# Optimization experiments

Hardware: AMD Instinct MI355X
Metric: run time of the kernel (lower is better)

Reference implementation:

```python
import jax, jax.numpy as jnp
import numpy as np

B, T, C, HS = 4, 2048, 1024, 128

def setup_inputs() -> dict:
    key = jax.random.key(0)
    k0, k1, k2, k3 = jax.random.split(key, 4)
    scale = 1.0 / np.sqrt(C)
    return {
        "x": jax.random.normal(k0, (B, T, C), dtype=jnp.float32),
        "Wk": jax.random.normal(k1, (C, HS), dtype=jnp.float32) * scale,
        "Wq": jax.random.normal(k2, (C, HS), dtype=jnp.float32) * scale,
        "Wv": jax.random.normal(k3, (C, HS), dtype=jnp.float32) * scale,
    }

def reference(x, Wk, Wq, Wv):
    # k, q, v: [B, T, HS]
    k = jnp.einsum('btc,ch->bth', x, Wk)
    q = jnp.einsum('btc,ch->bth', x, Wq)
    v = jnp.einsum('btc,ch->bth', x, Wv)
    hs = k.shape[-1]
    # full T x T scores (no causal mask in source), scaled by head_size**-0.5
    wei = jnp.einsum('bqh,bkh->bqk', q, k) * (hs ** -0.5)
    wei = jax.nn.softmax(wei, axis=-1)
    # dropout p=0.0 -> identity
    out = jnp.einsum('bqk,bkh->bqh', wei, v)
    return out
```

## Files before the change

kernel.cpp:

```cpp
#include <hip/hip_runtime.h>
#include <hip/hip_bf16.h>

typedef float  f32x4  __attribute__((ext_vector_type(4)));
typedef float  f32x8  __attribute__((ext_vector_type(8)));
typedef float  f32x16 __attribute__((ext_vector_type(16)));
typedef short  s4v    __attribute__((ext_vector_type(4)));
typedef short  s8v    __attribute__((ext_vector_type(8)));
typedef __bf16 b4v    __attribute__((ext_vector_type(4)));
typedef __bf16 b8v    __attribute__((ext_vector_type(8)));
typedef unsigned int u32;
typedef unsigned short ushort;

#define T_DIM  2048
#define C_DIM  1024


typedef const __attribute__((address_space(1))) u32 gu32;
typedef __attribute__((address_space(3))) u32 lu32;

static __device__ __forceinline__ void glds16(const void* g, void* l) {
  __builtin_amdgcn_global_load_lds((gu32*)g, (lu32*)l, 16, 0, 0);
}

static __device__ __forceinline__ b8v ldb8(const ushort* p) {
  return __builtin_bit_cast(b8v, *reinterpret_cast<const s8v*>(p));
}

static __device__ __forceinline__ b4v cvt4(f32x4 v) {
  b4v r;
#pragma unroll
  for (int i = 0; i < 4; ++i) r[i] = (__bf16)v[i];
  return r;
}

static __device__ __forceinline__ ushort bfu(float f) {
  __bf16 h = (__bf16)f;
  return __builtin_bit_cast(ushort, h);
}

static __device__ __forceinline__ f32x16 mfma32(b8v a, b8v b, f32x16 c) {
  return __builtin_amdgcn_mfma_f32_32x32x16_bf16(a, b, c, 0, 0, 0);
}

#define BAR_VM(N)                                                        \
  asm volatile("s_waitcnt vmcnt(" #N ") lgkmcnt(0)" ::: "memory");       \
  __builtin_amdgcn_s_barrier();                                          \
  asm volatile("" ::: "memory");

__global__ __launch_bounds__(256) void wconv(const float* __restrict__ Wq,
                                             const float* __restrict__ Wk,
                                             const float* __restrict__ Wv,
                                             ushort* __restrict__ Wt) {
  __shared__ float lds[32][65];
  const int m  = blockIdx.z;
  const int c0 = blockIdx.x * 32;
  const int h0 = blockIdx.y * 64;
  const float* W = (m == 0) ? Wq : (m == 1) ? Wk : Wv;

  const int cl = threadIdx.x >> 3;
  const int h8 = (threadIdx.x & 7) * 8;
  {
    float4 a = *reinterpret_cast<const float4*>(W + (c0 + cl) * 128 + h0 + h8);
    float4 b =
        *reinterpret_cast<const float4*>(W + (c0 + cl) * 128 + h0 + h8 + 4);
    lds[cl][h8] = a.x; lds[cl][h8 + 1] = a.y;
    lds[cl][h8 + 2] = a.z; lds[cl][h8 + 3] = a.w;
    lds[cl][h8 + 4] = b.x; lds[cl][h8 + 5] = b.y;
    lds[cl][h8 + 6] = b.z; lds[cl][h8 + 7] = b.w;
  }
  __syncthreads();
  const int hl = threadIdx.x >> 2;
  const int cs = (threadIdx.x & 3) * 8;
  s8v o;
#pragma unroll
  for (int i = 0; i < 8; ++i) o[i] = (short)bfu(lds[cs + i][hl]);
  *reinterpret_cast<s8v*>(Wt + (m * 128 + h0 + hl) * C_DIM + c0 + cs) = o;
}

__global__ __launch_bounds__(512) void proj(const float* __restrict__ x,
                                            const ushort* __restrict__ Wt,
                                            ushort* __restrict__ q,
                                            ushort* __restrict__ k,
                                            ushort* __restrict__ vt) {
  __shared__ __align__(16) ushort Ab[2][32 * 72];
  __shared__ __align__(16) ushort Bb[2][128 * 64];
  float* red = (float*)&Bb[0][0];
  ushort* stage = &Bb[1][0];

  const int t   = threadIdx.x;
  const int w   = t >> 6;
  const int lid = t & 63;
  const int hi  = lid >> 5;
  const int ln  = lid & 31;
  const int ks  = w >> 2;
  const int nc  = w & 3;
  const int m   = blockIdx.y;
  const int r0  = blockIdx.x * 32;

  const int arow = t >> 4;
  const int acol = (t & 15) * 4;
  const float* ag = x + (r0 + arow) * C_DIM + acol;

  const int bswz = (((lid & 7) ^ (lid >> 3)) << 4);
  const char* bg = (const char*)(Wt + m * 128 * C_DIM);

  f32x16 acc[2] = {};

#define PROJ_BSTAGE(KK, BUF)                                              \
  _Pragma("unroll") for (int j = 0; j < 2; ++j) {                         \
    int h = j * 64 + w * 8 + (lid >> 3);                                  \
    glds16(bg + h * 2048 + (KK) * 2 + bswz,                               \
           (char*)&Bb[BUF][0] + j * 8192 + w * 1024);                     \
  }

  f32x4 av = *reinterpret_cast<const f32x4*>(ag);
  PROJ_BSTAGE(0, 0)
  {
    b4v ac = cvt4(av);
    *reinterpret_cast<s4v*>(&Ab[0][arow * 72 + acol]) =
        __builtin_bit_cast(s4v, ac);
  }
  __syncthreads();

  int cur = 0;
#pragma unroll 1
  for (int i = 0; i < 16; ++i) {
    const int nxt = cur ^ 1;
    f32x4 an;
    if (i < 15) {
      const int kk = (i + 1) * 64;
      PROJ_BSTAGE(kk, nxt)
      an = *reinterpret_cast<const f32x4*>(ag + kk);
    }

    const int h = nc * 32 + ln;
#pragma unroll
    for (int c = 0; c < 2; ++c) {
      const int s = ks * 2 + c;
      b8v af = ldb8(&Ab[cur][ln * 72 + s * 16 + hi * 8]);
      int inner = ((s * 2 + hi) << 4) ^ ((h & 7) << 4);
      b8v bf =
          ldb8((const ushort*)((const char*)&Bb[cur][0] + h * 128 + inner));
      __builtin_amdgcn_s_setprio(1);
      acc[c] = mfma32(af, bf, acc[c]);
      __builtin_amdgcn_s_setprio(0);
    }

    if (i < 15) {
      b4v anc = cvt4(an);
      *reinterpret_cast<s4v*>(&Ab[nxt][arow * 72 + acol]) =
          __builtin_bit_cast(s4v, anc);
    }
    __syncthreads();
    cur = nxt;
  }
#undef PROJ_BSTAGE

  f32x16 fa = acc[0] + acc[1];

  if (ks == 1) {
#pragma unroll
    for (int r = 0; r < 16; ++r) {
      int qm = (r & 3) + 8 * (r >> 2) + 4 * hi;
      red[(nc * 32 + qm) * 32 + ln] = fa[r];
    }
  }
  __syncthreads();
  if (ks == 0) {
#pragma unroll
    for (int r = 0; r < 16; ++r) {
      int qm = (r & 3) + 8 * (r >> 2) + 4 * hi;
      fa[r] += red[(nc * 32 + qm) * 32 + ln];
    }
    if (m < 2) {
#pragma unroll
      for (int r = 0; r < 16; ++r) {
        int row = (r & 3) + 8 * (r >> 2) + 4 * hi;
        stage[row * 136 + nc * 32 + ln] = bfu(fa[r]);
      }
    } else {
#pragma unroll
      for (int r = 0; r < 16; ++r) {
        int trow = (r & 3) + 8 * (r >> 2) + 4 * hi;
        stage[(nc * 32 + ln) * 40 + trow] = bfu(fa[r]);
      }
    }
  }
  __syncthreads();

  if (m < 2) {
    ushort* dst = (m == 0) ? q : k;
    int row = t >> 4, col8 = t & 15;
    s8v v8 = *reinterpret_cast<const s8v*>(&stage[row * 136 + col8 * 8]);
    *reinterpret_cast<s8v*>(&dst[(r0 + row) * 128 + col8 * 8]) = v8;
  } else {
    int b = blockIdx.x >> 6;
    int tbase = (blockIdx.x & 63) * 32;
    int h2 = t >> 2, t8 = t & 3;
    s8v v8 = *reinterpret_cast<const s8v*>(&stage[h2 * 40 + t8 * 8]);
    *reinterpret_cast<s8v*>(&vt[(b * 128 + h2) * T_DIM + tbase + t8 * 8]) = v8;
  }
}

#define ATTN_STAGE(KV0, BUF)                                              \
  _Pragma("unroll") for (int j = 0; j < 4; ++j) {                         \
    int row = w * 16 + j * 4 + (lid >> 4);                                \
    int p_ = (row >> 2) & 7;                                              \
    int pg = (p_ & 4) | ((p_ & 1) << 1) | ((p_ >> 1) & 1);                \
    int srow = (row & ~31) | (pg << 2) | (row & 3);                       \
    glds16(kgb + ((KV0) + srow) * 256 + (((lid & 15) ^ (row & 15)) << 4), \
           smem + (BUF) * 65536 + w * 4096 + j * 1024);                   \
  }                                                                       \
  _Pragma("unroll") for (int j = 0; j < 4; ++j) {                         \
    int h = w * 16 + j * 4 + (lid >> 4);                                  \
    glds16(vgb + h * 4096 + (KV0) * 2 + (((lid & 15) ^ (h & 15)) << 4),   \
           smem + (BUF) * 65536 + 32768 + w * 4096 + j * 1024);           \
  }

#define ATTN2_QK(BUF)                                                    \
  {                                                                      \
    const char* Tb = smem + (BUF) * 65536;                               \
    b8v kfr[8];                                                          \
    _Pragma("unroll") for (int s = 0; s < 8; ++s)                        \
        kfr[s] = ldb8((const ushort*)(Tb + koff[s]));                    \
    f32x16 S = {};                                                       \
    __builtin_amdgcn_s_setprio(1);                                       \
    _Pragma("unroll") for (int s = 0; s < 8; ++s)                        \
        S = mfma32(kfr[s], aq[s], S);                                    \
    __builtin_amdgcn_s_setprio(0);                                       \
    float p[16];                                                         \
    _Pragma("unroll") for (int r = 0; r < 16; ++r) {                     \
      p[r] = __expf(S[r] * scale - 4.0f);                                \
      lsum += p[r];                                                      \
    }                                                                    \
    _Pragma("unroll") for (int r = 0; r < 8; ++r) {                      \
      pk0[r] = (__bf16)p[r];                                             \
      pk1[r] = (__bf16)p[8 + r];                                         \
    }                                                                    \
  }

#define ATTN2_PV(BUF)                                                   \
  {                                                                     \
    const char* Tb = smem + (BUF) * 65536;                              \
    __builtin_amdgcn_s_setprio(1);                                      \
    _Pragma("unroll") for (int ht = 0; ht < 4; ++ht) {                  \
      b8v v0 = ldb8((const ushort*)(Tb + voff[ht][0]));                 \
      b8v v1 = ldb8((const ushort*)(Tb + voff[ht][1]));                 \
      of[ht] = mfma32(pk0, v0, of[ht]);                                 \
      of[ht] = mfma32(pk1, v1, of[ht]);                                 \
    }                                                                   \
    __builtin_amdgcn_s_setprio(0);                                      \
  }

__global__ __launch_bounds__(512) void attn2(const ushort* __restrict__ q,
                                             const ushort* __restrict__ k,
                                             const ushort* __restrict__ vt,
                                             float* __restrict__ out,
                                             float* __restrict__ parts,
                                             float* __restrict__ lps) {
  extern __shared__ __align__(16) char smem[];

  const int t   = threadIdx.x;
  const int w   = t >> 6;
  const int lid = t & 63;
  const int hi  = lid >> 5;
  const int ln  = lid & 31;
  const int wq  = w >> 2;
  const int wk  = w & 3;

  const int id = blockIdx.x;
  const int g  = id & 7;
  const int b  = g >> 1;
  const int z  = g & 1;
  const int t0 = (id >> 3) * 64;

  const ushort* qp = q + (b * T_DIM + t0 + wq * 32) * 128;
  b8v aq[8];
#pragma unroll
  for (int s = 0; s < 8; ++s)
    aq[s] = ldb8(&qp[ln * 128 + s * 16 + hi * 8]);

  const char* kgb = (const char*)(k + b * T_DIM * 128);
  const char* vgb = (const char*)(vt + b * 128 * T_DIM);
  const int kv_base = z * 1024;

  const int R = wk * 32 + ln;
  int koff[8];
#pragma unroll
  for (int s = 0; s < 8; ++s)
    koff[s] = R * 256 + (((s * 2 + hi) ^ (R & 15)) << 4);
  int voff[4][2];
#pragma unroll
  for (int ht = 0; ht < 4; ++ht)
#pragma unroll
    for (int s = 0; s < 2; ++s) {
      int Hrow = ht * 32 + ln;
      int chunk = wk * 4 + s * 2 + hi;
      voff[ht][s] = 32768 + Hrow * 256 + ((chunk ^ (Hrow & 15)) << 4);
    }

  f32x16 of[4] = {};
  float lsum = 0.0f;
  b8v pk0, pk1;
  const float scale = 0.08838834764831845f;

  ATTN_STAGE(kv_base, 0)

#pragma unroll 1
  for (int i = 0; i < 7; ++i) {
    BAR_VM(4)
    ATTN_STAGE(kv_base + (i + 1) * 128, (i + 1) & 1)
    ATTN2_QK(i & 1)
    BAR_VM(8)
    ATTN2_PV(i & 1)
  }
  BAR_VM(4)
  ATTN2_QK(1)
  BAR_VM(0)
  ATTN2_PV(1)

  lsum += __shfl_xor(lsum, 32);

  __syncthreads();

  float* ob = (float*)smem;
  float* lb = (float*)(smem + 98304);

  if (lid < 32) lb[(wq * 4 + wk) * 32 + lid] = lsum;
  if (wk != 0) {
#pragma unroll
    for (int ht = 0; ht < 4; ++ht)
#pragma unroll
      for (int r = 0; r < 16; ++r) {
        int qm = (r & 3) + 8 * (r >> 2) + 4 * hi;
        ob[((wk - 1) * 64 + wq * 32 + qm) * 128 + ht * 32 + ln] = of[ht][r];
      }
  }
  __syncthreads();
  if (wk == 0) {
    float* dsto = (z == 0) ? out : parts;
#pragma unroll
    for (int ht = 0; ht < 4; ++ht)
#pragma unroll
      for (int r = 0; r < 16; ++r) {
        int qm = (r & 3) + 8 * (r >> 2) + 4 * hi;
        int row = wq * 32 + qm;
        int col = ht * 32 + ln;
        float val = of[ht][r] + ob[(0 * 64 + row) * 128 + col] +
                    ob[(1 * 64 + row) * 128 + col] +
                    ob[(2 * 64 + row) * 128 + col];
        dsto[(b * T_DIM + t0 + row) * 128 + col] = val;
      }
    if (lid < 32) {
      float lt = lb[(wq * 4 + 0) * 32 + lid] + lb[(wq * 4 + 1) * 32 + lid] +
                 lb[(wq * 4 + 2) * 32 + lid] + lb[(wq * 4 + 3) * 32 + lid];
      lps[z * 8192 + b * T_DIM + t0 + wq * 32 + lid] = lt;
    }
  }
}

__global__ __launch_bounds__(512) void attn3(const ushort* __restrict__ q,
                                             const ushort* __restrict__ k,
                                             const ushort* __restrict__ vt,
                                             float* __restrict__ out,
                                             float* __restrict__ parts,
                                             float* __restrict__ lps) {
  extern __shared__ __align__(16) char smem[];

  const int t   = threadIdx.x;
  const int w   = t >> 6;
  const int lid = t & 63;
  const int hi  = lid >> 5;
  const int ln  = lid & 31;
  const int wq  = w >> 2;
  const int wh  = (w >> 1) & 1;
  const int wk  = w & 1;
  const int b   = blockIdx.y;
  const int z   = blockIdx.z;
  const int t0  = blockIdx.x * 64;

  const ushort* qp = q + (b * T_DIM + t0 + wq * 32) * 128;
  b8v aq[8];
#pragma unroll
  for (int s = 0; s < 8; ++s)
    aq[s] = ldb8(&qp[ln * 128 + s * 16 + hi * 8]);

  const char* kgb = (const char*)(k + b * T_DIM * 128);
  const char* vgb = (const char*)(vt + b * 128 * T_DIM);
  const int kv_base = z * 512;

  const int R = wk * 32 + ln;
  int koff[8];
#pragma unroll
  for (int s = 0; s < 8; ++s)
    koff[s] = R * 256 + (((s * 2 + hi) ^ (R & 15)) << 4);
  int voff[2][2];
#pragma unroll
  for (int ht = 0; ht < 2; ++ht)
#pragma unroll
    for (int s = 0; s < 2; ++s) {
      int Hrow = wh * 64 + ht * 32 + ln;
      int chunk = wk * 4 + s * 2 + hi;
      voff[ht][s] = 16384 + Hrow * 128 + ((chunk ^ (Hrow & 7)) << 4);
    }

  f32x16 of[2] = {};
  float lsum = 0.0f;
  b8v pk0, pk1;
  const float scale = 0.08838834764831845f;

#define A3_STAGE(KV0, BUF)                                                \
  _Pragma("unroll") for (int j = 0; j < 2; ++j) {                         \
    int row = (w * 2 + j) * 4 + (lid >> 4);                               \
    int p_ = (row >> 2) & 7;                                              \
    int pg = (p_ & 4) | ((p_ & 1) << 1) | ((p_ >> 1) & 1);                \
    int srow = (row & ~31) | (pg << 2) | (row & 3);                       \
    glds16(kgb + ((KV0) + srow) * 256 + (((lid & 15) ^ (row & 15)) << 4), \
           smem + (BUF) * 32768 + (w * 2 + j) * 1024);                    \
  }                                                                       \
  _Pragma("unroll") for (int j = 0; j < 2; ++j) {                         \
    int h = (w * 2 + j) * 8 + (lid >> 3);                                 \
    glds16(vgb + h * 4096 + (KV0) * 2 + (((lid & 7) ^ (h & 7)) << 4),     \
           smem + (BUF) * 32768 + 16384 + (w * 2 + j) * 1024);            \
  }

#define A3_QK(BUF)                                                       \
  {                                                                      \
    const char* Tb = smem + (BUF) * 32768;                               \
    b8v kfr[8];                                                          \
    _Pragma("unroll") for (int s = 0; s < 8; ++s)                        \
        kfr[s] = ldb8((const ushort*)(Tb + koff[s]));                    \
    f32x16 S = {};                                                       \
    __builtin_amdgcn_s_setprio(1);                                       \
    _Pragma("unroll") for (int s = 0; s < 8; ++s)                        \
        S = mfma32(kfr[s], aq[s], S);                                    \
    __builtin_amdgcn_s_setprio(0);                                       \
    float p[16];                                                         \
    _Pragma("unroll") for (int r = 0; r < 16; ++r) {                     \
      p[r] = __expf(S[r] * scale - 4.0f);                                \
      lsum += p[r];                                                      \
    }                                                                    \
    _Pragma("unroll") for (int r = 0; r < 8; ++r) {                      \
      pk0[r] = (__bf16)p[r];                                             \
      pk1[r] = (__bf16)p[8 + r];                                         \
    }                                                                    \
  }

#define A3_PV(BUF)                                                      \
  {                                                                     \
    const char* Tb = smem + (BUF) * 32768;                              \
    __builtin_amdgcn_s_setprio(1);                                      \
    _Pragma("unroll") for (int ht = 0; ht < 2; ++ht) {                  \
      b8v v0 = ldb8((const ushort*)(Tb + voff[ht][0]));                 \
      b8v v1 = ldb8((const ushort*)(Tb + voff[ht][1]));                 \
      of[ht] = mfma32(pk0, v0, of[ht]);                                 \
      of[ht] = mfma32(pk1, v1, of[ht]);                                 \
    }                                                                   \
    __builtin_amdgcn_s_setprio(0);                                      \
  }

  A3_STAGE(kv_base, 0)

#pragma unroll 1
  for (int i = 0; i < 7; ++i) {
    BAR_VM(2)
    A3_STAGE(kv_base + (i + 1) * 64, (i + 1) & 1)
    A3_QK(i & 1)
    BAR_VM(4)
    A3_PV(i & 1)
  }
  BAR_VM(2)
  A3_QK(1)
  BAR_VM(0)
  A3_PV(1)

#undef A3_STAGE
#undef A3_QK
#undef A3_PV

  lsum += __shfl_xor(lsum, 32);

  __syncthreads();

  float* ob = (float*)smem;
  float* lb = (float*)(smem + 32768);

  if (wh == 0 && lid < 32) lb[(wk * 2 + wq) * 32 + lid] = lsum;
  if (wk == 1) {
#pragma unroll
    for (int ht = 0; ht < 2; ++ht)
#pragma unroll
      for (int r = 0; r < 16; ++r) {
        int qm = (r & 3) + 8 * (r >> 2) + 4 * hi;
        ob[(wq * 2 + wh) * 2048 + qm * 64 + ht * 32 + ln] = of[ht][r];
      }
  }
  __syncthreads();
  if (wk == 0) {
    float* dsto = (z == 0) ? out : (parts + (z - 1) * 1048576);
#pragma unroll
    for (int ht = 0; ht < 2; ++ht)
#pragma unroll
      for (int r = 0; r < 16; ++r) {
        int qm = (r & 3) + 8 * (r >> 2) + 4 * hi;
        int row = wq * 32 + qm;
        int col = wh * 64 + ht * 32 + ln;
        float val = of[ht][r] + ob[(wq * 2 + wh) * 2048 + qm * 64 + ht * 32 + ln];
        dsto[(b * T_DIM + t0 + row) * 128 + col] = val;
      }
    if (wh == 0 && lid < 32) {
      float lt = lb[(0 * 2 + wq) * 32 + lid] + lb[(1 * 2 + wq) * 32 + lid];
      lps[z * 8192 + b * T_DIM + t0 + wq * 32 + lid] = lt;
    }
  }
}

__global__ __launch_bounds__(256) void fin(float* __restrict__ out,
                                           const float* __restrict__ parts,
                                           const float* __restrict__ lps,
                                           int nz) {
  int tid = blockIdx.x * 256 + threadIdx.x;
  int idx = tid * 4;
  int row = idx >> 7;
  float l = lps[row];
  for (int zz = 1; zz < nz; ++zz) l += lps[zz * 8192 + row];
  float inv = 1.0f / l;
  f32x4 a = *reinterpret_cast<const f32x4*>(out + idx);
  for (int zz = 1; zz < nz; ++zz) {
    f32x4 c = *reinterpret_cast<const f32x4*>(parts + (zz - 1) * 1048576 + idx);
    a += c;
  }
  f32x4 r;
#pragma unroll
  for (int i = 0; i < 4; ++i) r[i] = a[i] * inv;
  *reinterpret_cast<f32x4*>(out + idx) = r;
}

extern "C" void kernel_launch(void* const* d_in, const int* in_sizes, int n_in,
                              void* d_out, int out_size, void* d_ws,
                              size_t ws_size, hipStream_t stream) {
  const float* x  = (const float*)d_in[0];
  const float* Wk = (const float*)d_in[1];
  const float* Wq = (const float*)d_in[2];
  const float* Wv = (const float*)d_in[3];
  float* out = (float*)d_out;

  char* ws = (char*)d_ws;
  ushort* Wt  = (ushort*)ws;
  ushort* qb  = (ushort*)(ws + 786432);
  ushort* kb  = (ushort*)(ws + 2883584);
  ushort* vtb = (ushort*)(ws + 4980736);
  float* parts = (float*)(ws + 7077888);

  const bool big = ws_size >= 19800000u;
  float* lps = big ? (float*)(ws + 7077888 + 3u * 4194304u)
                   : (float*)(ws + 7077888 + 4194304u);

  (void)hipFuncSetAttribute(reinterpret_cast<const void*>(&attn2),
                            hipFuncAttributeMaxDynamicSharedMemorySize, 131072);
  (void)hipFuncSetAttribute(reinterpret_cast<const void*>(&attn3),
                            hipFuncAttributeMaxDynamicSharedMemorySize, 65536);

  wconv<<<dim3(32, 2, 3), dim3(256), 0, stream>>>(Wq, Wk, Wv, Wt);
  proj<<<dim3(256, 3), dim3(512), 0, stream>>>(x, Wt, qb, kb, vtb);
  if (big) {
    attn3<<<dim3(32, 4, 4), dim3(512), 65536, stream>>>(qb, kb, vtb, out,
                                                        parts, lps);
    fin<<<dim3(1024), dim3(256), 0, stream>>>(out, parts, lps, 4);
  } else {
    attn2<<<dim3(256), dim3(512), 131072, stream>>>(qb, kb, vtb, out,
                                                    parts, lps);
    fin<<<dim3(1024), dim3(256), 0, stream>>>(out, parts, lps, 2);
  }
}
```

Before: 55.11 us.

## Store split-KV partials as bf16 and simplify attention pipeline waits

```diff
diff --git a/kernel.cpp b/kernel.cpp
--- a/kernel.cpp
+++ b/kernel.cpp
@@ -36,6 +36,11 @@
 static __device__ __forceinline__ ushort bfu(float f) {
   __bf16 h = (__bf16)f;
   return __builtin_bit_cast(ushort, h);
+}
+
+static __device__ __forceinline__ float b2f(ushort u) {
+  u32 x = ((u32)u) << 16;
+  return __builtin_bit_cast(float, x);
 }
 
 static __device__ __forceinline__ f32x16 mfma32(b8v a, b8v b, f32x16 c) {
@@ -217,7 +222,58 @@
            smem + (BUF) * 65536 + 32768 + w * 4096 + j * 1024);           \
   }
 
-#define ATTN2_QK(BUF)                                                    \
+__global__ __launch_bounds__(512) void attn2(const ushort* __restrict__ q,
+                                             const ushort* __restrict__ k,
+                                             const ushort* __restrict__ vt,
+                                             float* __restrict__ out,
+                                             float* __restrict__ parts,
+                                             float* __restrict__ lps) {
+  extern __shared__ __align__(16) char smem[];
+
+  const int t   = threadIdx.x;
+  const int w   = t >> 6;
+  const int lid = t & 63;
+  const int hi  = lid >> 5;
+  const int ln  = lid & 31;
+  const int wq  = w >> 2;
+  const int wk  = w & 3;
+
+  const int id = blockIdx.x;
+  const int g  = id & 7;
+  const int b  = g >> 1;
+  const int z  = g & 1;
+  const int t0 = (id >> 3) * 64;
+
+  const ushort* qp = q + (b * T_DIM + t0 + wq * 32) * 128;
+  b8v aq[8];
+#pragma unroll
+  for (int s = 0; s < 8; ++s)
+    aq[s] = ldb8(&qp[ln * 128 + s * 16 + hi * 8]);
+
+  const char* kgb = (const char*)(k + b * T_DIM * 128);
+  const char* vgb = (const char*)(vt + b * 128 * T_DIM);
+  const int kv_base = z * 1024;
+
+  const int R = wk * 32 + ln;
+  int koff[8];
+#pragma unroll
+  for (int s = 0; s < 8; ++s)
+    koff[s] = R * 256 + (((s * 2 + hi) ^ (R & 15)) << 4);
+  int voff[4][2];
+#pragma unroll
+  for (int ht = 0; ht < 4; ++ht)
+#pragma unroll
+    for (int s = 0; s < 2; ++s) {
+      int Hrow = ht * 32 + ln;
+      int chunk = wk * 4 + s * 2 + hi;
+      voff[ht][s] = 32768 + Hrow * 256 + ((chunk ^ (Hrow & 15)) << 4);
+    }
+
+  f32x16 of[4] = {};
+  float lsum = 0.0f;
+  const float scale = 0.08838834764831845f;
+
+#define ATTN2_BODY(BUF)                                                  \
   {                                                                      \
     const char* Tb = smem + (BUF) * 65536;                               \
     b8v kfr[8];                                                          \
@@ -233,91 +289,30 @@
       p[r] = __expf(S[r] * scale - 4.0f);                                \
       lsum += p[r];                                                      \
     }                                                                    \
+    b8v pk0, pk1;                                                        \
     _Pragma("unroll") for (int r = 0; r < 8; ++r) {                      \
       pk0[r] = (__bf16)p[r];                                             \
       pk1[r] = (__bf16)p[8 + r];                                         \
     }                                                                    \
-  }
-
-#define ATTN2_PV(BUF)                                                   \
-  {                                                                     \
-    const char* Tb = smem + (BUF) * 65536;                              \
-    __builtin_amdgcn_s_setprio(1);                                      \
-    _Pragma("unroll") for (int ht = 0; ht < 4; ++ht) {                  \
-      b8v v0 = ldb8((const ushort*)(Tb + voff[ht][0]));                 \
-      b8v v1 = ldb8((const ushort*)(Tb + voff[ht][1]));                 \
-      of[ht] = mfma32(pk0, v0, of[ht]);                                 \
-      of[ht] = mfma32(pk1, v1, of[ht]);                                 \
-    }                                                                   \
-    __builtin_amdgcn_s_setprio(0);                                      \
-  }
-
-__global__ __launch_bounds__(512) void attn2(const ushort* __restrict__ q,
-                                             const ushort* __restrict__ k,
-                                             const ushort* __restrict__ vt,
-                                             float* __restrict__ out,
-                                             float* __restrict__ parts,
-                                             float* __restrict__ lps) {
-  extern __shared__ __align__(16) char smem[];
-
-  const int t   = threadIdx.x;
-  const int w   = t >> 6;
-  const int lid = t & 63;
-  const int hi  = lid >> 5;
-  const int ln  = lid & 31;
-  const int wq  = w >> 2;
-  const int wk  = w & 3;
-
-  const int id = blockIdx.x;
-  const int g  = id & 7;
-  const int b  = g >> 1;
-  const int z  = g & 1;
-  const int t0 = (id >> 3) * 64;
-
-  const ushort* qp = q + (b * T_DIM + t0 + wq * 32) * 128;
-  b8v aq[8];
-#pragma unroll
-  for (int s = 0; s < 8; ++s)
-    aq[s] = ldb8(&qp[ln * 128 + s * 16 + hi * 8]);
-
-  const char* kgb = (const char*)(k + b * T_DIM * 128);
-  const char* vgb = (const char*)(vt + b * 128 * T_DIM);
-  const int kv_base = z * 1024;
-
-  const int R = wk * 32 + ln;
-  int koff[8];
-#pragma unroll
-  for (int s = 0; s < 8; ++s)
-    koff[s] = R * 256 + (((s * 2 + hi) ^ (R & 15)) << 4);
-  int voff[4][2];
-#pragma unroll
-  for (int ht = 0; ht < 4; ++ht)
-#pragma unroll
-    for (int s = 0; s < 2; ++s) {
-      int Hrow = ht * 32 + ln;
-      int chunk = wk * 4 + s * 2 + hi;
-      voff[ht][s] = 32768 + Hrow * 256 + ((chunk ^ (Hrow & 15)) << 4);
-    }
-
-  f32x16 of[4] = {};
-  float lsum = 0.0f;
-  b8v pk0, pk1;
-  const float scale = 0.08838834764831845f;
+    __builtin_amdgcn_s_setprio(1);                                       \
+    _Pragma("unroll") for (int ht = 0; ht < 4; ++ht) {                   \
+      b8v v0 = ldb8((const ushort*)(Tb + voff[ht][0]));                  \
+      b8v v1 = ldb8((const ushort*)(Tb + voff[ht][1]));                  \
+      of[ht] = mfma32(pk0, v0, of[ht]);                                  \
+      of[ht] = mfma32(pk1, v1, of[ht]);                                  \
+    }                                                                    \
+    __builtin_amdgcn_s_setprio(0);                                       \
+  }
 
   ATTN_STAGE(kv_base, 0)
 
 #pragma unroll 1
-  for (int i = 0; i < 7; ++i) {
-    BAR_VM(4)
-    ATTN_STAGE(kv_base + (i + 1) * 128, (i + 1) & 1)
-    ATTN2_QK(i & 1)
-    BAR_VM(8)
-    ATTN2_PV(i & 1)
-  }
-  BAR_VM(4)
-  ATTN2_QK(1)
-  BAR_VM(0)
-  ATTN2_PV(1)
+  for (int i = 0; i < 8; ++i) {
+    BAR_VM(0)
+    if (i < 7) { ATTN_STAGE(kv_base + (i + 1) * 128, (i + 1) & 1) }
+    ATTN2_BODY(i & 1)
+  }
+#undef ATTN2_BODY
 
   lsum += __shfl_xor(lsum, 32);
 
@@ -363,7 +358,7 @@
                                              const ushort* __restrict__ k,
                                              const ushort* __restrict__ vt,
                                              float* __restrict__ out,
-                                             float* __restrict__ parts,
+                                             ushort* __restrict__ parts16,
                                              float* __restrict__ lps) {
   extern __shared__ __align__(16) char smem[];
 
@@ -406,7 +401,6 @@
 
   f32x16 of[2] = {};
   float lsum = 0.0f;
-  b8v pk0, pk1;
   const float scale = 0.08838834764831845f;
 
 #define A3_STAGE(KV0, BUF)                                                \
@@ -424,7 +418,7 @@
            smem + (BUF) * 32768 + 16384 + (w * 2 + j) * 1024);            \
   }
 
-#define A3_QK(BUF)                                                       \
+#define A3_BODY(BUF)                                                     \
   {                                                                      \
     const char* Tb = smem + (BUF) * 32768;                               \
     b8v kfr[8];                                                          \
@@ -440,43 +434,31 @@
       p[r] = __expf(S[r] * scale - 4.0f);                                \
       lsum += p[r];                                                      \
     }                                                                    \
+    b8v pk0, pk1;                                                        \
     _Pragma("unroll") for (int r = 0; r < 8; ++r) {                      \
       pk0[r] = (__bf16)p[r];                                             \
       pk1[r] = (__bf16)p[8 + r];                                         \
     }                                                                    \
-  }
-
-#define A3_PV(BUF)                                                      \
-  {                                                                     \
-    const char* Tb = smem + (BUF) * 32768;                              \
-    __builtin_amdgcn_s_setprio(1);                                      \
-    _Pragma("unroll") for (int ht = 0; ht < 2; ++ht) {                  \
-      b8v v0 = ldb8((const ushort*)(Tb + voff[ht][0]));                 \
-      b8v v1 = ldb8((const ushort*)(Tb + voff[ht][1]));                 \
-      of[ht] = mfma32(pk0, v0, of[ht]);                                 \
-      of[ht] = mfma32(pk1, v1, of[ht]);                                 \
-    }                                                                   \
-    __builtin_amdgcn_s_setprio(0);                                      \
+    __builtin_amdgcn_s_setprio(1);                                       \
+    _Pragma("unroll") for (int ht = 0; ht < 2; ++ht) {                   \
+      b8v v0 = ldb8((const ushort*)(Tb + voff[ht][0]));                  \
+      b8v v1 = ldb8((const ushort*)(Tb + voff[ht][1]));                  \
+      of[ht] = mfma32(pk0, v0, of[ht]);                                  \
+      of[ht] = mfma32(pk1, v1, of[ht]);                                  \
+    }                                                                    \
+    __builtin_amdgcn_s_setprio(0);                                       \
   }
 
   A3_STAGE(kv_base, 0)
 
 #pragma unroll 1
-  for (int i = 0; i < 7; ++i) {
-    BAR_VM(2)
-    A3_STAGE(kv_base + (i + 1) * 64, (i + 1) & 1)
-    A3_QK(i & 1)
-    BAR_VM(4)
-    A3_PV(i & 1)
-  }
-  BAR_VM(2)
-  A3_QK(1)
-  BAR_VM(0)
-  A3_PV(1)
-
+  for (int i = 0; i < 8; ++i) {
+    BAR_VM(0)
+    if (i < 7) { A3_STAGE(kv_base + (i + 1) * 64, (i + 1) & 1) }
+    A3_BODY(i & 1)
+  }
 #undef A3_STAGE
-#undef A3_QK
-#undef A3_PV
+#undef A3_BODY
 
   lsum += __shfl_xor(lsum, 32);
 
@@ -497,7 +479,6 @@
   }
   __syncthreads();
   if (wk == 0) {
-    float* dsto = (z == 0) ? out : (parts + (z - 1) * 1048576);
 #pragma unroll
     for (int ht = 0; ht < 2; ++ht)
 #pragma unroll
@@ -505,8 +486,13 @@
         int qm = (r & 3) + 8 * (r >> 2) + 4 * hi;
         int row = wq * 32 + qm;
         int col = wh * 64 + ht * 32 + ln;
-        float val = of[ht][r] + ob[(wq * 2 + wh) * 2048 + qm * 64 + ht * 32 + ln];
-        dsto[(b * T_DIM + t0 + row) * 128 + col] = val;
+        float val =
+            of[ht][r] + ob[(wq * 2 + wh) * 2048 + qm * 64 + ht * 32 + ln];
+        long idx = (long)(b * T_DIM + t0 + row) * 128 + col;
+        if (z == 0)
+          out[idx] = val;
+        else
+          parts16[(long)(z - 1) * 1048576 + idx] = bfu(val);
       }
     if (wh == 0 && lid < 32) {
       float lt = lb[(0 * 2 + wq) * 32 + lid] + lb[(1 * 2 + wq) * 32 + lid];
@@ -517,18 +503,33 @@
 
 __global__ __launch_bounds__(256) void fin(float* __restrict__ out,
                                            const float* __restrict__ parts,
-                                           const float* __restrict__ lps,
-                                           int nz) {
+                                           const float* __restrict__ lps) {
   int tid = blockIdx.x * 256 + threadIdx.x;
   int idx = tid * 4;
   int row = idx >> 7;
-  float l = lps[row];
-  for (int zz = 1; zz < nz; ++zz) l += lps[zz * 8192 + row];
+  float inv = 1.0f / (lps[row] + lps[8192 + row]);
+  f32x4 a = *reinterpret_cast<const f32x4*>(out + idx);
+  f32x4 c = *reinterpret_cast<const f32x4*>(parts + idx);
+  f32x4 r;
+#pragma unroll
+  for (int i = 0; i < 4; ++i) r[i] = (a[i] + c[i]) * inv;
+  *reinterpret_cast<f32x4*>(out + idx) = r;
+}
+
+__global__ __launch_bounds__(256) void fin4(float* __restrict__ out,
+                                            const ushort* __restrict__ parts16,
+                                            const float* __restrict__ lps) {
+  int tid = blockIdx.x * 256 + threadIdx.x;
+  int idx = tid * 4;
+  int row = idx >> 7;
+  float l = lps[row] + lps[8192 + row] + lps[16384 + row] + lps[24576 + row];
   float inv = 1.0f / l;
   f32x4 a = *reinterpret_cast<const f32x4*>(out + idx);
-  for (int zz = 1; zz < nz; ++zz) {
-    f32x4 c = *reinterpret_cast<const f32x4*>(parts + (zz - 1) * 1048576 + idx);
-    a += c;
+#pragma unroll
+  for (int zz = 0; zz < 3; ++zz) {
+    s4v u = *reinterpret_cast<const s4v*>(parts16 + (long)zz * 1048576 + idx);
+#pragma unroll
+    for (int i = 0; i < 4; ++i) a[i] += b2f((ushort)u[i]);
   }
   f32x4 r;
 #pragma unroll
@@ -546,30 +547,38 @@
   float* out = (float*)d_out;
 
   char* ws = (char*)d_ws;
-  ushort* Wt  = (ushort*)ws;
-  ushort* qb  = (ushort*)(ws + 786432);
-  ushort* kb  = (ushort*)(ws + 2883584);
-  ushort* vtb = (ushort*)(ws + 4980736);
-  float* parts = (float*)(ws + 7077888);
-
-  const bool big = ws_size >= 19800000u;
-  float* lps = big ? (float*)(ws + 7077888 + 3u * 4194304u)
-                   : (float*)(ws + 7077888 + 4194304u);
+  const bool big = ws_size >= 13500416u;
 
   (void)hipFuncSetAttribute(reinterpret_cast<const void*>(&attn2),
                             hipFuncAttributeMaxDynamicSharedMemorySize, 131072);
   (void)hipFuncSetAttribute(reinterpret_cast<const void*>(&attn3),
                             hipFuncAttributeMaxDynamicSharedMemorySize, 65536);
 
-  wconv<<<dim3(32, 2, 3), dim3(256), 0, stream>>>(Wq, Wk, Wv, Wt);
-  proj<<<dim3(256, 3), dim3(512), 0, stream>>>(x, Wt, qb, kb, vtb);
   if (big) {
+    ushort* Wt  = (ushort*)ws;
+    ushort* qb  = (ushort*)(ws + 786432);
+    ushort* kb  = (ushort*)(ws + 2883584);
+    ushort* vtb = (ushort*)(ws + 4980736);
+    ushort* parts16 = (ushort*)(ws + 7077888);
+    float* lps = (float*)(ws + 13369344);
+
+    wconv<<<dim3(32, 2, 3), dim3(256), 0, stream>>>(Wq, Wk, Wv, Wt);
+    proj<<<dim3(256, 3), dim3(512), 0, stream>>>(x, Wt, qb, kb, vtb);
     attn3<<<dim3(32, 4, 4), dim3(512), 65536, stream>>>(qb, kb, vtb, out,
-                                                        parts, lps);
-    fin<<<dim3(1024), dim3(256), 0, stream>>>(out, parts, lps, 4);
+                                                        parts16, lps);
+    fin4<<<dim3(1024), dim3(256), 0, stream>>>(out, parts16, lps);
   } else {
+    ushort* Wt  = (ushort*)ws;
+    ushort* qb  = (ushort*)(ws + (1u << 20));
+    ushort* kb  = (ushort*)(ws + 3u * (1u << 20));
+    ushort* vtb = (ushort*)(ws + 5u * (1u << 20));
+    float* parts = (float*)(ws + 8u * (1u << 20));
+    float* lps   = (float*)(ws + 12u * (1u << 20));
+
+    wconv<<<dim3(32, 2, 3), dim3(256), 0, stream>>>(Wq, Wk, Wv, Wt);
+    proj<<<dim3(256, 3), dim3(512), 0, stream>>>(x, Wt, qb, kb, vtb);
     attn2<<<dim3(256), dim3(512), 131072, stream>>>(qb, kb, vtb, out,
                                                     parts, lps);
-    fin<<<dim3(1024), dim3(256), 0, stream>>>(out, parts, lps, 2);
-  }
-}
+    fin<<<dim3(1024), dim3(256), 0, stream>>>(out, parts, lps);
+  }
+}
```

New measurement: 55.95 us. Within noise of the previous version (+1.5%).
